# Kernel optimization log

Hardware: AMD Instinct MI355X
Metric: run time of the kernel (lower is better)

Reference implementation:

```python
import jax, jax.numpy as jnp
import numpy as np

B, T_AUDIO, D_IN = 64, 500, 768
H = 1024
NUM_CHARS = 1024  # must equal H: one-hot char embeddings feed the LSTM input
SEQ_LEN = 128


def setup_inputs() -> dict:
    key = jax.random.key(0)
    ks = jax.random.split(key, 16)
    s = 1.0 / np.sqrt(H)
    u = lambda k, shape: jax.random.uniform(k, shape, jnp.float32, -s, s)
    return {
        "audio_features": jax.random.normal(ks[0], (B, T_AUDIO, D_IN), jnp.float32),
        "text_indices": jax.random.randint(ks[1], (B, SEQ_LEN), 0, NUM_CHARS),
        "W_proj": u(ks[2], (H, D_IN)), "b_proj": u(ks[3], (H,)),
        "W_ih0": u(ks[4], (4 * H, H)), "W_hh0": u(ks[5], (4 * H, H)),
        "b_ih0": u(ks[6], (4 * H,)), "b_hh0": u(ks[7], (4 * H,)),
        "W_ih1": u(ks[8], (4 * H, H)), "W_hh1": u(ks[9], (4 * H, H)),
        "b_ih1": u(ks[10], (4 * H,)), "b_hh1": u(ks[11], (4 * H,)),
        "W_out": u(ks[12], (NUM_CHARS, H)), "b_out": u(ks[13], (NUM_CHARS,)),
    }


def _lstm_cell(x, h, c, W_ih, W_hh, b_ih, b_hh):
    # PyTorch gate order: i, f, g, o
    g = x @ W_ih.T + h @ W_hh.T + b_ih + b_hh
    i, f, gg, o = jnp.split(g, 4, axis=-1)
    c = jax.nn.sigmoid(f) * c + jax.nn.sigmoid(i) * jnp.tanh(gg)
    h = jax.nn.sigmoid(o) * jnp.tanh(c)
    return h, c


def reference(audio_features, text_indices, W_proj, b_proj,
              W_ih0, W_hh0, b_ih0, b_hh0,
              W_ih1, W_hh1, b_ih1, b_hh1,
              W_out, b_out):
    # audio encoding: project then mean-pool over time -> [B, H]
    audio_enc = jnp.mean(audio_features @ W_proj.T + b_proj, axis=1)
    seq_len = text_indices.shape[1]
    # teacher-forcing inputs: step 0 = audio encoding, steps 1..L-1 = one-hot of
    # text_indices[:, 1:seq_len-1] (NUM_CHARS == H)
    one_hots = jax.nn.one_hot(text_indices[:, 1:seq_len - 1], NUM_CHARS,
                              dtype=audio_enc.dtype)  # [B, L-1, H]
    xs = jnp.concatenate([audio_enc[:, None, :], one_hots], axis=1)  # [B, L, H]
    xs = jnp.swapaxes(xs, 0, 1)  # [L, B, H]
    z = jnp.zeros((audio_enc.shape[0], H), audio_enc.dtype)

    def step(carry, x):
        h0, c0, h1, c1 = carry
        h0, c0 = _lstm_cell(x, h0, c0, W_ih0, W_hh0, b_ih0, b_hh0)
        h1, c1 = _lstm_cell(h0, h1, c1, W_ih1, W_hh1, b_ih1, b_hh1)
        return (h0, c0, h1, c1), h1

    _, hs = jax.lax.scan(step, (z, z, z, z), xs)  # hs: [L, B, H]
    outs = jnp.swapaxes(hs, 0, 1)  # [B, L, H]
    logits = outs @ W_out.T + b_out  # [B, L, NUM_CHARS]
    return logits
```

## Files before the change

kernel.cpp:

```cpp
#include <hip/hip_runtime.h>
#include <hip/hip_bf16.h>

#define HH     1024
#define BB     64
#define DIN    768
#define TAUD   500
#define LSTEPS 127
#define G4     4096
#define NB     256
#define BHH    (BB*HH)
#define GST    17

typedef __attribute__((ext_vector_type(8))) short bf16x8;
typedef __attribute__((ext_vector_type(4))) float f32x4;
typedef unsigned short u16;
typedef unsigned long long u64;

__device__ __forceinline__ u16 f2b(float x){
  __hip_bfloat16 h = __float2bfloat16(x);
  return __builtin_bit_cast(u16, h);
}
__device__ __forceinline__ float b2f(u16 u){
  unsigned int x = ((unsigned int)u) << 16;
  return __builtin_bit_cast(float, x);
}
__device__ __forceinline__ float sig_(float x){ return 1.0f/(1.0f+__expf(-x)); }
__device__ __forceinline__ float tanh_(float x){
  float ax = fabsf(x);
  float e  = __expf(-2.0f*ax);
  float t  = (1.0f-e)/(1.0f+e);
  return x < 0.0f ? -t : t;
}

constexpr size_t O_PACK  = 0;
constexpr size_t O_WOHI  = O_PACK + (size_t)NB*4*16384*2;
constexpr size_t O_WOLO  = O_WOHI + (size_t)HH*HH*2;
constexpr size_t O_B0P   = O_WOLO + (size_t)HH*HH*2;
constexpr size_t O_B1P   = O_B0P  + G4*4;
constexpr size_t O_MEAN  = O_B1P  + G4*4;
constexpr size_t O_X0    = O_MEAN + (size_t)BB*DIN*4;
constexpr size_t O_H0    = O_X0   + (size_t)BHH*2;
constexpr size_t O_H1    = O_H0   + (size_t)2*BHH*2;
constexpr size_t O_HS    = O_H1   + (size_t)2*BHH*2;
constexpr size_t O_BAR   = O_HS   + (size_t)LSTEPS*BHH*2;

__global__ void init_kernel(u16* h0, u16* h1, int* bar){
  int i = blockIdx.x*256 + threadIdx.x;
  int st = gridDim.x*256;
  for (int k=i;k<2*BHH;k+=st){ h0[k]=0; h1[k]=0; }
  if (i < 512) bar[i] = 0;
}

__global__ void pool_kernel(const float* __restrict__ audio, float* __restrict__ mean){
  int b = blockIdx.x/3, dc = blockIdx.x%3;
  int d = dc*256 + threadIdx.x;
  const float* p = audio + (size_t)b*TAUD*DIN + d;
  float s = 0.f;
  #pragma unroll 5
  for (int t=0;t<TAUD;++t) s += p[(size_t)t*DIN];
  mean[b*DIN + d] = s*(1.0f/TAUD);
}

__global__ void project_kernel(const float* __restrict__ mean, const float* __restrict__ Wp,
                               const float* __restrict__ bp, u16* __restrict__ x0){
  __shared__ float wrow[DIN];
  __shared__ float part[256];
  int h = blockIdx.x;
  for (int i=threadIdx.x;i<DIN;i+=256) wrow[i] = Wp[(size_t)h*DIN + i];
  __syncthreads();
  int b = threadIdx.x>>2, q = threadIdx.x&3;
  const float* mr = mean + b*DIN + q*192;
  const float* wr = wrow + q*192;
  float s = 0.f;
  #pragma unroll 8
  for (int i=0;i<192;++i) s += mr[i]*wr[i];
  part[threadIdx.x] = s;
  __syncthreads();
  if (q==0){
    float v = part[threadIdx.x]+part[threadIdx.x+1]+part[threadIdx.x+2]+part[threadIdx.x+3] + bp[h];
    x0[b*HH + h] = f2b(v);
  }
}

__global__ void pack_w_kernel(const float* __restrict__ Wih0, const float* __restrict__ Whh0,
                              const float* __restrict__ Wih1, const float* __restrict__ Whh1,
                              u16* __restrict__ P){
  int bid = blockIdx.x, m = blockIdx.y;
  const float* src = (m==0)? Wih0 : (m==1)? Whh0 : (m==2)? Wih1 : Whh1;
  u16* dst = P + ((size_t)bid*4 + m)*16384;
  for (int e = threadIdx.x; e < 16384; e += 256){
    int r = e&31, col = (e>>5)&15, ktg = e>>9;
    int ng = bid*4 + (col&3) + (col>>2)*HH;
    dst[e] = f2b(src[(size_t)ng*HH + ktg*32 + r]);
  }
}

__global__ void pack_bias_kernel(const float* bih0, const float* bhh0,
                                 const float* bih1, const float* bhh1,
                                 float* B0p, float* B1p){
  int i = blockIdx.x*256 + threadIdx.x;
  if (i < G4){
    int n = (i>>2) + (i&3)*HH;
    B0p[i] = bih0[n]+bhh0[n];
    B1p[i] = bih1[n]+bhh1[n];
  }
}

__global__ void wout_kernel(const float* __restrict__ src, u16* __restrict__ hi,
                            u16* __restrict__ lo, int n){
  int i = blockIdx.x*256+threadIdx.x, st = gridDim.x*256;
  for (;i<n;i+=st){
    float v = src[i];
    u16 h = f2b(v);
    hi[i] = h;
    lo[i] = f2b(v - b2f(h));
  }
}

__device__ __forceinline__ void sysst32(unsigned* p, unsigned v){
  __hip_atomic_store(p, v, __ATOMIC_RELAXED, __HIP_MEMORY_SCOPE_SYSTEM);
}

__device__ __forceinline__ void gridbar(int* bar, int t){
  __syncthreads();
  if (threadIdx.x==0){
    int leaf = blockIdx.x>>4;
    int a = __hip_atomic_fetch_add(&bar[leaf*32], 1, __ATOMIC_RELAXED, __HIP_MEMORY_SCOPE_SYSTEM);
    int r = a - t*16;
    if (r == 15)
      __hip_atomic_fetch_add(&bar[511], 1, __ATOMIC_RELAXED, __HIP_MEMORY_SCOPE_SYSTEM);
    if (r == 0 || r == 15){
      while (__hip_atomic_load(&bar[511], __ATOMIC_RELAXED, __HIP_MEMORY_SCOPE_SYSTEM) < (t+1)*16)
        __builtin_amdgcn_s_sleep(4);
      if (r == 0)
        __hip_atomic_store(&bar[leaf*32+16], t+1, __ATOMIC_RELAXED, __HIP_MEMORY_SCOPE_SYSTEM);
    } else {
      while (__hip_atomic_load(&bar[leaf*32+16], __ATOMIC_RELAXED, __HIP_MEMORY_SCOPE_SYSTEM) < t+1)
        __builtin_amdgcn_s_sleep(4);
    }
    asm volatile("" ::: "memory");
  }
  __syncthreads();
  if (threadIdx.x < 64)
    __builtin_amdgcn_fence(__ATOMIC_ACQUIRE, "agent");
  __syncthreads();
}

__device__ __forceinline__ f32x4 gemm1(const u16* __restrict__ A, const u16* B, f32x4 acc){
  bf16x8 af[16];
  #pragma unroll
  for (int kt=0;kt<16;++kt) af[kt] = *(const bf16x8*)(A + kt*32);
  #pragma unroll
  for (int kt=0;kt<16;++kt){
    bf16x8 b = *(const bf16x8*)(B + kt*512);
    acc = __builtin_amdgcn_mfma_f32_16x16x32_bf16(af[kt], b, acc, 0, 0, 0);
  }
  return acc;
}
__device__ __forceinline__ f32x4 gemm2(const u16* __restrict__ A1, const u16* __restrict__ A2,
                                       const u16* B1, const u16* B2, f32x4 acc){
  bf16x8 af[16], ag[16];
  #pragma unroll
  for (int kt=0;kt<16;++kt) af[kt] = *(const bf16x8*)(A1 + kt*32);
  #pragma unroll
  for (int kt=0;kt<16;++kt) ag[kt] = *(const bf16x8*)(A2 + kt*32);
  #pragma unroll
  for (int kt=0;kt<16;++kt)
    acc = __builtin_amdgcn_mfma_f32_16x16x32_bf16(af[kt], *(const bf16x8*)(B1 + kt*512), acc, 0,0,0);
  #pragma unroll
  for (int kt=0;kt<16;++kt)
    acc = __builtin_amdgcn_mfma_f32_16x16x32_bf16(ag[kt], *(const bf16x8*)(B2 + kt*512), acc, 0,0,0);
  return acc;
}

__global__ void __launch_bounds__(512, 2) lstm_kernel(
    const u16* __restrict__ P, const float* __restrict__ B0p,
    const float* __restrict__ B1p, const u16* __restrict__ x0bf,
    const int* __restrict__ tix,
    u16* __restrict__ h0bf, u16* __restrict__ h1bf,
    u16* __restrict__ hs, int* __restrict__ bar)
{
  extern __shared__ char smem[];
  u16*   Plds  = (u16*)smem;
  float* gates = (float*)(smem + 131072);
  u16*   tixl  = (u16*)(smem + 131072 + 8704);

  const int tid  = threadIdx.x;
  const int lane = tid&63, w = tid>>6, quad = lane>>4, colc = lane&15;
  const int mg   = w>>1, kh = w&1;
  const int bid  = blockIdx.x;

  {
    const bf16x8* gs = (const bf16x8*)(P + (size_t)bid*65536);
    bf16x8* gd = (bf16x8*)Plds;
    #pragma unroll
    for (int i=0;i<16;++i) gd[tid + i*512] = gs[tid + i*512];
    for (int i=tid; i<BB*128; i+=512) tixl[i] = (u16)tix[(i&63)*128 + (i>>6)];
  }

  const int aoff = (mg*16 + colc)*HH + kh*512 + quad*8;
  const int boff = kh*8192 + colc*32 + quad*8;

  const int cb = tid>>2, cjj = tid&3;
  float cc0 = 0.f, cc1 = 0.f;
  float4 vb0 = {0,0,0,0}, vb1 = {0,0,0,0};
  if (tid < 256){
    vb0 = *(const float4*)(B0p + (bid*4+cjj)*4);
    vb1 = *(const float4*)(B1p + (bid*4+cjj)*4);
  }
  __syncthreads();

  #pragma unroll 1
  for (int t=0;t<LSTEPS;++t){
    const int cur = t&1, nxt = cur^1;
    {
      const u16* Ab = ((t==0)? x0bf : (h0bf + (size_t)cur*BHH)) + aoff;
      const u16* Bb = Plds + ((t==0)? 0 : 16384) + boff;
      f32x4 z = {0.f,0.f,0.f,0.f};
      f32x4 acc = gemm1(Ab, Bb, z);
      __syncthreads();
      #pragma unroll
      for (int r=0;r<4;++r) gates[(kh*64 + mg*16 + quad*4 + r)*GST + colc] = acc[r];
    }
    __syncthreads();
    if (tid < 256){
      float gv[4];
      #pragma unroll
      for (int g=0;g<4;++g)
        gv[g] = gates[cb*GST + g*4+cjj] + gates[(64+cb)*GST + g*4+cjj];
      gv[0]+=vb0.x; gv[1]+=vb0.y; gv[2]+=vb0.z; gv[3]+=vb0.w;
      if (t>0){
        int ch = tixl[t*64 + cb];
        int base = (ch>>5)*512 + (ch&31);
        #pragma unroll
        for (int g=0;g<4;++g) gv[g] += b2f(Plds[base + (g*4+cjj)*32]);
      }
      cc0 = sig_(gv[1])*cc0 + sig_(gv[0])*tanh_(gv[2]);
      float hn = sig_(gv[3])*tanh_(cc0);
      unsigned hv = f2b(hn);
      unsigned ov = __shfl_xor(hv, 1);
      if ((cjj&1)==0)
        sysst32((unsigned*)(h0bf + (size_t)nxt*BHH) + (cb*HH + bid*4 + cjj)/2, hv | (ov<<16));
    }
    gridbar(bar, t);
    {
      f32x4 z = {0.f,0.f,0.f,0.f};
      f32x4 acc = gemm2(h0bf + (size_t)nxt*BHH + aoff, h1bf + (size_t)cur*BHH + aoff,
                        Plds + 2*16384 + boff,         Plds + 3*16384 + boff, z);
      #pragma unroll
      for (int r=0;r<4;++r) gates[(kh*64 + mg*16 + quad*4 + r)*GST + colc] = acc[r];
    }
    __syncthreads();
    if (tid < 256){
      float gv[4];
      #pragma unroll
      for (int g=0;g<4;++g)
        gv[g] = gates[cb*GST + g*4+cjj] + gates[(64+cb)*GST + g*4+cjj];
      gv[0]+=vb1.x; gv[1]+=vb1.y; gv[2]+=vb1.z; gv[3]+=vb1.w;
      cc1 = sig_(gv[1])*cc1 + sig_(gv[0])*tanh_(gv[2]);
      float hn = sig_(gv[3])*tanh_(cc1);
      unsigned hv = f2b(hn);
      unsigned ov = __shfl_xor(hv, 1);
      if ((cjj&1)==0){
        sysst32((unsigned*)(h1bf + (size_t)nxt*BHH) + (cb*HH + bid*4 + cjj)/2, hv | (ov<<16));
        sysst32((unsigned*)hs + (((size_t)t*BB + cb)*HH + bid*4 + cjj)/2, hv | (ov<<16));
      }
    }
  }
}

__global__ void __launch_bounds__(512) logits_kernel(
    const u16* __restrict__ hs, const u16* __restrict__ Whi, const u16* __restrict__ Wlo,
    const float* __restrict__ bout, float* __restrict__ out)
{
  extern __shared__ u16 bsh[];
  const int tid = threadIdx.x;
  const int w = tid>>6, lane = tid&63, quad = lane>>4, col = lane&15;
  const int mt = blockIdx.x*8 + w;
  const bool active = (mt < (LSTEPS*BB)/16);
  bf16x8 afr[32];
  if (active){
    const u16* ap = hs + (size_t)(mt*16+col)*HH + quad*8;
    #pragma unroll
    for (int kt=0;kt<32;++kt) afr[kt] = *(const bf16x8*)(ap + kt*32);
  }
  const int nt0 = blockIdx.y*16;
  for (int nt=nt0; nt<nt0+16; ++nt){
    __syncthreads();
    #pragma unroll
    for (int i=0;i<8;++i){
      int cid = i*512 + tid;
      int mat = cid>>11;
      int r = (cid>>7)&15, ck = cid&127;
      const u16* src = (mat? Wlo : Whi) + (size_t)(nt*16+r)*HH + ck*8;
      *(bf16x8*)(bsh + mat*16512 + r*1032 + ck*8) = *(const bf16x8*)src;
    }
    __syncthreads();
    if (active){
      f32x4 acc = {0.f,0.f,0.f,0.f};
      const u16* bh = bsh + col*1032 + quad*8;
      const u16* bl = bsh + 16512 + col*1032 + quad*8;
      #pragma unroll 8
      for (int kt=0;kt<32;++kt){
        bf16x8 b1 = *(const bf16x8*)(bh + kt*32);
        acc = __builtin_amdgcn_mfma_f32_16x16x32_bf16(afr[kt], b1, acc, 0,0,0);
        bf16x8 b2 = *(const bf16x8*)(bl + kt*32);
        acc = __builtin_amdgcn_mfma_f32_16x16x32_bf16(afr[kt], b2, acc, 0,0,0);
      }
      float bb = bout[nt*16 + col];
      #pragma unroll
      for (int r=0;r<4;++r){
        int m = mt*16 + quad*4 + r;
        int tt = m>>6, b_ = m&63;
        out[((size_t)b_*LSTEPS + tt)*HH + nt*16 + col] = acc[r] + bb;
      }
    }
  }
}

extern "C" void kernel_launch(void* const* d_in, const int* in_sizes, int n_in,
                              void* d_out, int out_size, void* d_ws, size_t ws_size,
                              hipStream_t stream) {
  const float* audio = (const float*)d_in[0];
  const int*   tix   = (const int*)  d_in[1];
  const float* Wproj = (const float*)d_in[2];
  const float* bproj = (const float*)d_in[3];
  const float* Wih0  = (const float*)d_in[4];
  const float* Whh0  = (const float*)d_in[5];
  const float* bih0  = (const float*)d_in[6];
  const float* bhh0  = (const float*)d_in[7];
  const float* Wih1  = (const float*)d_in[8];
  const float* Whh1  = (const float*)d_in[9];
  const float* bih1  = (const float*)d_in[10];
  const float* bhh1  = (const float*)d_in[11];
  const float* Wout  = (const float*)d_in[12];
  const float* bout  = (const float*)d_in[13];
  float* out = (float*)d_out;

  char* ws = (char*)d_ws;
  u16*   wP    = (u16*)  (ws + O_PACK);
  u16*   wWoHi = (u16*)  (ws + O_WOHI);
  u16*   wWoLo = (u16*)  (ws + O_WOLO);
  float* wB0p  = (float*)(ws + O_B0P);
  float* wB1p  = (float*)(ws + O_B1P);
  float* wMean = (float*)(ws + O_MEAN);
  u16*   wX0   = (u16*)  (ws + O_X0);
  u16*   wH0   = (u16*)  (ws + O_H0);
  u16*   wH1   = (u16*)  (ws + O_H1);
  u16*   wHS   = (u16*)  (ws + O_HS);
  int*   wBar  = (int*)  (ws + O_BAR);

  init_kernel<<<64, 256, 0, stream>>>(wH0, wH1, wBar);
  pool_kernel<<<BB*3, 256, 0, stream>>>(audio, wMean);
  project_kernel<<<HH, 256, 0, stream>>>(wMean, Wproj, bproj, wX0);
  pack_w_kernel<<<dim3(NB,4), 256, 0, stream>>>(Wih0, Whh0, Wih1, Whh1, wP);
  pack_bias_kernel<<<16, 256, 0, stream>>>(bih0, bhh0, bih1, bhh1, wB0p, wB1p);
  wout_kernel<<<512, 256, 0, stream>>>(Wout, wWoHi, wWoLo, HH*HH);
  lstm_kernel<<<NB, 512, 131072 + 8704 + 16384, stream>>>(
      wP, wB0p, wB1p, wX0, tix, wH0, wH1, wHS, wBar);
  logits_kernel<<<dim3(64,4), 512, 66048, stream>>>(wHS, wWoHi, wWoLo, bout, out);
}
```

Before: 2.521 ms.

## Restructure LSTM step loop: one grid barrier per step, shuffle-based gate transpose

Layer 0's first step (the audio input) is now computed before the loop in a separate g0 kernel. Its input-weight matrix is repacked into a gather table, so one-hot inputs become an LDS lookup. The step loop is reordered so layer-1 step t and layer-0 step t+1 both follow a single grid barrier, which removes one barrier per step. Blocks drop to 256 threads with full-K MFMA per wave, and the gate transpose uses lane shuffles instead of LDS round trips and __syncthreads. The costs are longer per-wave dependent MFMA chains, less parallelism per block, and an extra precompute kernel.

```diff
diff --git a/kernel.cpp b/kernel.cpp
--- a/kernel.cpp
+++ b/kernel.cpp
@@ -9,7 +9,6 @@
 #define G4     4096
 #define NB     256
 #define BHH    (BB*HH)
-#define GST    17
 
 typedef __attribute__((ext_vector_type(8))) short bf16x8;
 typedef __attribute__((ext_vector_type(4))) float f32x4;
@@ -33,11 +32,13 @@
 }
 
 constexpr size_t O_PACK  = 0;
-constexpr size_t O_WOHI  = O_PACK + (size_t)NB*4*16384*2;
+constexpr size_t O_WG    = O_PACK + (size_t)NB*3*16384*2;
+constexpr size_t O_WOHI  = O_WG   + (size_t)NB*16384*2;
 constexpr size_t O_WOLO  = O_WOHI + (size_t)HH*HH*2;
 constexpr size_t O_B0P   = O_WOLO + (size_t)HH*HH*2;
 constexpr size_t O_B1P   = O_B0P  + G4*4;
-constexpr size_t O_MEAN  = O_B1P  + G4*4;
+constexpr size_t O_G0    = O_B1P  + G4*4;
+constexpr size_t O_MEAN  = O_G0   + (size_t)BB*HH*4*4;
 constexpr size_t O_X0    = O_MEAN + (size_t)BB*DIN*4;
 constexpr size_t O_H0    = O_X0   + (size_t)BHH*2;
 constexpr size_t O_H1    = O_H0   + (size_t)2*BHH*2;
@@ -82,16 +83,54 @@
   }
 }
 
-__global__ void pack_w_kernel(const float* __restrict__ Wih0, const float* __restrict__ Whh0,
-                              const float* __restrict__ Wih1, const float* __restrict__ Whh1,
-                              u16* __restrict__ P){
+__global__ void g0_kernel(const float* __restrict__ Wih0, const u16* __restrict__ x0bf,
+                          float* __restrict__ G0p){
+  __shared__ float wr[4][HH];
+  __shared__ float part[256][4];
+  int u = blockIdx.x;
+  for (int i=threadIdx.x; i<4*HH; i+=256){
+    int g = i>>10, k = i&1023;
+    wr[g][k] = b2f(f2b(Wih0[(size_t)(u + g*HH)*HH + k]));
+  }
+  __syncthreads();
+  int b = threadIdx.x>>2, q = threadIdx.x&3;
+  const u16* xr = x0bf + b*HH + q*256;
+  float s0=0,s1=0,s2=0,s3=0;
+  for (int k=0;k<256;++k){
+    float xv = b2f(xr[k]);
+    s0 += xv*wr[0][q*256+k]; s1 += xv*wr[1][q*256+k];
+    s2 += xv*wr[2][q*256+k]; s3 += xv*wr[3][q*256+k];
+  }
+  part[threadIdx.x][0]=s0; part[threadIdx.x][1]=s1;
+  part[threadIdx.x][2]=s2; part[threadIdx.x][3]=s3;
+  __syncthreads();
+  if (threadIdx.x < 64){
+    int bb = threadIdx.x;
+    #pragma unroll
+    for (int g=0;g<4;++g){
+      float v = part[bb*4][g]+part[bb*4+1][g]+part[bb*4+2][g]+part[bb*4+3][g];
+      G0p[((size_t)bb*HH + u)*4 + g] = v;
+    }
+  }
+}
+
+__global__ void pack_w_kernel(const float* __restrict__ Whh0, const float* __restrict__ Wih1,
+                              const float* __restrict__ Whh1, u16* __restrict__ P){
   int bid = blockIdx.x, m = blockIdx.y;
-  const float* src = (m==0)? Wih0 : (m==1)? Whh0 : (m==2)? Wih1 : Whh1;
-  u16* dst = P + ((size_t)bid*4 + m)*16384;
+  const float* src = (m==0)? Whh0 : (m==1)? Wih1 : Whh1;
+  u16* dst = P + ((size_t)bid*3 + m)*16384;
   for (int e = threadIdx.x; e < 16384; e += 256){
     int r = e&31, col = (e>>5)&15, ktg = e>>9;
     int ng = bid*4 + (col&3) + (col>>2)*HH;
     dst[e] = f2b(src[(size_t)ng*HH + ktg*32 + r]);
+  }
+}
+
+__global__ void pack_wg_kernel(const float* __restrict__ Wih0, u16* __restrict__ WG){
+  int bid = blockIdx.x;
+  for (int i = threadIdx.x; i < 16384; i += 256){
+    int ch = i>>4, u = (i>>2)&3, g = i&3;
+    WG[(size_t)bid*16384 + i] = f2b(Wih0[(size_t)(bid*4 + u + g*HH)*HH + ch]);
   }
 }
 
@@ -146,125 +185,135 @@
   __syncthreads();
 }
 
-__device__ __forceinline__ f32x4 gemm1(const u16* __restrict__ A, const u16* B, f32x4 acc){
-  bf16x8 af[16];
+__device__ __forceinline__ f32x4 gemmK(const u16* __restrict__ A, const u16* B, f32x4 acc){
   #pragma unroll
-  for (int kt=0;kt<16;++kt) af[kt] = *(const bf16x8*)(A + kt*32);
+  for (int h=0; h<2; ++h){
+    bf16x8 af[16];
+    #pragma unroll
+    for (int i=0;i<16;++i) af[i] = *(const bf16x8*)(A + (h*16+i)*32);
+    #pragma unroll
+    for (int i=0;i<16;++i)
+      acc = __builtin_amdgcn_mfma_f32_16x16x32_bf16(af[i], *(const bf16x8*)(B + (h*16+i)*512), acc, 0,0,0);
+  }
+  return acc;
+}
+__device__ __forceinline__ f32x4 gemm2K(const u16* __restrict__ A1, const u16* __restrict__ A2,
+                                        const u16* B1, const u16* B2){
+  f32x4 a1 = {0,0,0,0}, a2 = {0,0,0,0};
   #pragma unroll
-  for (int kt=0;kt<16;++kt){
-    bf16x8 b = *(const bf16x8*)(B + kt*512);
-    acc = __builtin_amdgcn_mfma_f32_16x16x32_bf16(af[kt], b, acc, 0, 0, 0);
-  }
-  return acc;
-}
-__device__ __forceinline__ f32x4 gemm2(const u16* __restrict__ A1, const u16* __restrict__ A2,
-                                       const u16* B1, const u16* B2, f32x4 acc){
-  bf16x8 af[16], ag[16];
+  for (int h=0; h<2; ++h){
+    bf16x8 af[16], ag[16];
+    #pragma unroll
+    for (int i=0;i<16;++i) af[i] = *(const bf16x8*)(A1 + (h*16+i)*32);
+    #pragma unroll
+    for (int i=0;i<16;++i) ag[i] = *(const bf16x8*)(A2 + (h*16+i)*32);
+    #pragma unroll
+    for (int i=0;i<16;++i){
+      a1 = __builtin_amdgcn_mfma_f32_16x16x32_bf16(af[i], *(const bf16x8*)(B1 + (h*16+i)*512), a1, 0,0,0);
+      a2 = __builtin_amdgcn_mfma_f32_16x16x32_bf16(ag[i], *(const bf16x8*)(B2 + (h*16+i)*512), a2, 0,0,0);
+    }
+  }
+  return a1 + a2;
+}
+
+__device__ __forceinline__ void xpose(const f32x4 acc, float* gv, int lane){
+  const int base = lane & 48, up = (lane>>2)&3, r = lane&3;
   #pragma unroll
-  for (int kt=0;kt<16;++kt) af[kt] = *(const bf16x8*)(A1 + kt*32);
-  #pragma unroll
-  for (int kt=0;kt<16;++kt) ag[kt] = *(const bf16x8*)(A2 + kt*32);
-  #pragma unroll
-  for (int kt=0;kt<16;++kt)
-    acc = __builtin_amdgcn_mfma_f32_16x16x32_bf16(af[kt], *(const bf16x8*)(B1 + kt*512), acc, 0,0,0);
-  #pragma unroll
-  for (int kt=0;kt<16;++kt)
-    acc = __builtin_amdgcn_mfma_f32_16x16x32_bf16(ag[kt], *(const bf16x8*)(B2 + kt*512), acc, 0,0,0);
-  return acc;
-}
-
-__global__ void __launch_bounds__(512, 2) lstm_kernel(
-    const u16* __restrict__ P, const float* __restrict__ B0p,
-    const float* __restrict__ B1p, const u16* __restrict__ x0bf,
-    const int* __restrict__ tix,
+  for (int g=0; g<4; ++g){
+    int src = base | (g*4 + up);
+    float v0 = __shfl(acc[0], src);
+    float v1 = __shfl(acc[1], src);
+    float v2 = __shfl(acc[2], src);
+    float v3 = __shfl(acc[3], src);
+    gv[g] = (r==0)? v0 : (r==1)? v1 : (r==2)? v2 : v3;
+  }
+}
+
+__global__ void __launch_bounds__(256, 1) lstm_kernel(
+    const u16* __restrict__ P, const u16* __restrict__ WG,
+    const float* __restrict__ B0p, const float* __restrict__ B1p,
+    const float* __restrict__ G0p, const int* __restrict__ tix,
     u16* __restrict__ h0bf, u16* __restrict__ h1bf,
     u16* __restrict__ hs, int* __restrict__ bar)
 {
   extern __shared__ char smem[];
-  u16*   Plds  = (u16*)smem;
-  float* gates = (float*)(smem + 131072);
-  u16*   tixl  = (u16*)(smem + 131072 + 8704);
+  u16* Plds = (u16*)smem;
+  u16* WGl  = (u16*)(smem + 98304);
+  u16* tixl = (u16*)(smem + 98304 + 32768);
 
   const int tid  = threadIdx.x;
-  const int lane = tid&63, w = tid>>6, quad = lane>>4, colc = lane&15;
-  const int mg   = w>>1, kh = w&1;
+  const int lane = tid&63, mg = tid>>6, quad = lane>>4, colc = lane&15;
   const int bid  = blockIdx.x;
 
   {
-    const bf16x8* gs = (const bf16x8*)(P + (size_t)bid*65536);
+    const bf16x8* gs = (const bf16x8*)(P + (size_t)bid*49152);
     bf16x8* gd = (bf16x8*)Plds;
     #pragma unroll
-    for (int i=0;i<16;++i) gd[tid + i*512] = gs[tid + i*512];
-    for (int i=tid; i<BB*128; i+=512) tixl[i] = (u16)tix[(i&63)*128 + (i>>6)];
-  }
-
-  const int aoff = (mg*16 + colc)*HH + kh*512 + quad*8;
-  const int boff = kh*8192 + colc*32 + quad*8;
-
-  const int cb = tid>>2, cjj = tid&3;
+    for (int i=0;i<24;++i) gd[tid + i*256] = gs[tid + i*256];
+    const bf16x8* ws = (const bf16x8*)(WG + (size_t)bid*16384);
+    bf16x8* wd = (bf16x8*)WGl;
+    #pragma unroll
+    for (int i=0;i<8;++i) wd[tid + i*256] = ws[tid + i*256];
+    for (int i=tid; i<BB*128; i+=256) tixl[i] = (u16)tix[(i&63)*128 + (i>>6)];
+  }
+
+  const int aoff = (mg*16 + colc)*HH + quad*8;
+  const int boff = colc*32 + quad*8;
+  const u16* B_hh0 = Plds + boff;
+  const u16* B_ih1 = Plds + 16384 + boff;
+  const u16* B_hh1 = Plds + 2*16384 + boff;
+
+  const int bT = mg*16 + quad*4 + (lane&3);
+  const int up = (lane>>2)&3;
+  const int ug = bid*4 + up;
+  const float4 vb0 = *(const float4*)(B0p + ug*4);
+  const float4 vb1 = *(const float4*)(B1p + ug*4);
   float cc0 = 0.f, cc1 = 0.f;
-  float4 vb0 = {0,0,0,0}, vb1 = {0,0,0,0};
-  if (tid < 256){
-    vb0 = *(const float4*)(B0p + (bid*4+cjj)*4);
-    vb1 = *(const float4*)(B1p + (bid*4+cjj)*4);
-  }
-  __syncthreads();
+  __syncthreads();
+
+  {
+    float4 g0 = *(const float4*)(G0p + ((size_t)bT*HH + ug)*4);
+    float gi = g0.x+vb0.x, gf = g0.y+vb0.y, gg = g0.z+vb0.z, go = g0.w+vb0.w;
+    cc0 = sig_(gi)*tanh_(gg);
+    unsigned hv = f2b(sig_(go)*tanh_(cc0));
+    unsigned ov = __shfl_xor(hv, 4);
+    if ((lane&4)==0)
+      sysst32((unsigned*)(h0bf + (size_t)BHH) + (bT*HH + ug)/2, hv | (ov<<16));
+  }
 
   #pragma unroll 1
   for (int t=0;t<LSTEPS;++t){
     const int cur = t&1, nxt = cur^1;
-    {
-      const u16* Ab = ((t==0)? x0bf : (h0bf + (size_t)cur*BHH)) + aoff;
-      const u16* Bb = Plds + ((t==0)? 0 : 16384) + boff;
-      f32x4 z = {0.f,0.f,0.f,0.f};
-      f32x4 acc = gemm1(Ab, Bb, z);
-      __syncthreads();
-      #pragma unroll
-      for (int r=0;r<4;++r) gates[(kh*64 + mg*16 + quad*4 + r)*GST + colc] = acc[r];
-    }
-    __syncthreads();
-    if (tid < 256){
-      float gv[4];
-      #pragma unroll
-      for (int g=0;g<4;++g)
-        gv[g] = gates[cb*GST + g*4+cjj] + gates[(64+cb)*GST + g*4+cjj];
-      gv[0]+=vb0.x; gv[1]+=vb0.y; gv[2]+=vb0.z; gv[3]+=vb0.w;
-      if (t>0){
-        int ch = tixl[t*64 + cb];
-        int base = (ch>>5)*512 + (ch&31);
-        #pragma unroll
-        for (int g=0;g<4;++g) gv[g] += b2f(Plds[base + (g*4+cjj)*32]);
-      }
-      cc0 = sig_(gv[1])*cc0 + sig_(gv[0])*tanh_(gv[2]);
-      float hn = sig_(gv[3])*tanh_(cc0);
-      unsigned hv = f2b(hn);
-      unsigned ov = __shfl_xor(hv, 1);
-      if ((cjj&1)==0)
-        sysst32((unsigned*)(h0bf + (size_t)nxt*BHH) + (cb*HH + bid*4 + cjj)/2, hv | (ov<<16));
-    }
     gridbar(bar, t);
     {
-      f32x4 z = {0.f,0.f,0.f,0.f};
-      f32x4 acc = gemm2(h0bf + (size_t)nxt*BHH + aoff, h1bf + (size_t)cur*BHH + aoff,
-                        Plds + 2*16384 + boff,         Plds + 3*16384 + boff, z);
-      #pragma unroll
-      for (int r=0;r<4;++r) gates[(kh*64 + mg*16 + quad*4 + r)*GST + colc] = acc[r];
-    }
-    __syncthreads();
-    if (tid < 256){
+      f32x4 acc = gemm2K(h0bf + (size_t)nxt*BHH + aoff, h1bf + (size_t)cur*BHH + aoff,
+                         B_ih1, B_hh1);
       float gv[4];
-      #pragma unroll
-      for (int g=0;g<4;++g)
-        gv[g] = gates[cb*GST + g*4+cjj] + gates[(64+cb)*GST + g*4+cjj];
+      xpose(acc, gv, lane);
       gv[0]+=vb1.x; gv[1]+=vb1.y; gv[2]+=vb1.z; gv[3]+=vb1.w;
       cc1 = sig_(gv[1])*cc1 + sig_(gv[0])*tanh_(gv[2]);
-      float hn = sig_(gv[3])*tanh_(cc1);
-      unsigned hv = f2b(hn);
-      unsigned ov = __shfl_xor(hv, 1);
-      if ((cjj&1)==0){
-        sysst32((unsigned*)(h1bf + (size_t)nxt*BHH) + (cb*HH + bid*4 + cjj)/2, hv | (ov<<16));
-        sysst32((unsigned*)hs + (((size_t)t*BB + cb)*HH + bid*4 + cjj)/2, hv | (ov<<16));
+      unsigned hv = f2b(sig_(gv[3])*tanh_(cc1));
+      unsigned ov = __shfl_xor(hv, 4);
+      if ((lane&4)==0){
+        unsigned pk = hv | (ov<<16);
+        sysst32((unsigned*)(h1bf + (size_t)nxt*BHH) + (bT*HH + ug)/2, pk);
+        sysst32((unsigned*)hs + (((size_t)t*BB + bT)*HH + ug)/2, pk);
       }
+    }
+    if (t < LSTEPS-1){
+      f32x4 z = {0,0,0,0};
+      f32x4 acc = gemmK(h0bf + (size_t)nxt*BHH + aoff, B_hh0, z);
+      float gv[4];
+      xpose(acc, gv, lane);
+      int ch = tixl[(t+1)*64 + bT];
+      ushort4 wv = *(const ushort4*)(WGl + ch*16 + up*4);
+      gv[0]+=vb0.x+b2f(wv.x); gv[1]+=vb0.y+b2f(wv.y);
+      gv[2]+=vb0.z+b2f(wv.z); gv[3]+=vb0.w+b2f(wv.w);
+      cc0 = sig_(gv[1])*cc0 + sig_(gv[0])*tanh_(gv[2]);
+      unsigned hv = f2b(sig_(gv[3])*tanh_(cc0));
+      unsigned ov = __shfl_xor(hv, 4);
+      if ((lane&4)==0)
+        sysst32((unsigned*)(h0bf + (size_t)cur*BHH) + (bT*HH + ug)/2, hv | (ov<<16));
     }
   }
 }
@@ -339,10 +388,12 @@
 
   char* ws = (char*)d_ws;
   u16*   wP    = (u16*)  (ws + O_PACK);
+  u16*   wWG   = (u16*)  (ws + O_WG);
   u16*   wWoHi = (u16*)  (ws + O_WOHI);
   u16*   wWoLo = (u16*)  (ws + O_WOLO);
   float* wB0p  = (float*)(ws + O_B0P);
   float* wB1p  = (float*)(ws + O_B1P);
+  float* wG0   = (float*)(ws + O_G0);
   float* wMean = (float*)(ws + O_MEAN);
   u16*   wX0   = (u16*)  (ws + O_X0);
   u16*   wH0   = (u16*)  (ws + O_H0);
@@ -353,10 +404,12 @@
   init_kernel<<<64, 256, 0, stream>>>(wH0, wH1, wBar);
   pool_kernel<<<BB*3, 256, 0, stream>>>(audio, wMean);
   project_kernel<<<HH, 256, 0, stream>>>(wMean, Wproj, bproj, wX0);
-  pack_w_kernel<<<dim3(NB,4), 256, 0, stream>>>(Wih0, Whh0, Wih1, Whh1, wP);
+  g0_kernel<<<HH, 256, 0, stream>>>(Wih0, wX0, wG0);
+  pack_w_kernel<<<dim3(NB,3), 256, 0, stream>>>(Whh0, Wih1, Whh1, wP);
+  pack_wg_kernel<<<NB, 256, 0, stream>>>(Wih0, wWG);
   pack_bias_kernel<<<16, 256, 0, stream>>>(bih0, bhh0, bih1, bhh1, wB0p, wB1p);
   wout_kernel<<<512, 256, 0, stream>>>(Wout, wWoHi, wWoLo, HH*HH);
-  lstm_kernel<<<NB, 512, 131072 + 8704 + 16384, stream>>>(
-      wP, wB0p, wB1p, wX0, tix, wH0, wH1, wHS, wBar);
+  lstm_kernel<<<NB, 256, 98304 + 32768 + 16384, stream>>>(
+      wP, wWG, wB0p, wB1p, wG0, tix, wH0, wH1, wHS, wBar);
   logits_kernel<<<dim3(64,4), 512, 66048, stream>>>(wHS, wWoHi, wWoLo, bout, out);
 }
```

New measurement: 2.625 ms. 4.1% more time.
